# Kernel tuning notes

Hardware: AMD Instinct MI355X
Metric: run time of the kernel (lower is better)

Reference implementation:

```python
import jax, jax.numpy as jnp
from jax import lax
import numpy as np

GRID_SIZE = 3
SPLINE_ORDER = 2
N_BASIS = GRID_SIZE + SPLINE_ORDER  # 5
_H = 2.0 / GRID_SIZE  # grid_range [-1, 1]
# extended uniform grid, shape (1, grid_size + 2*spline_order + 1) = (1, 8)
GRID = (jnp.arange(-SPLINE_ORDER, GRID_SIZE + SPLINE_ORDER + 1, dtype=jnp.float32) * _H - 1.0)[None, :]


def b_splines(x):
    """Cox-de Boor B-spline bases. x: (..., F) -> (..., F, N_BASIS)."""
    x = x[..., None]
    g = GRID
    bases = ((x >= g[:, :-1]) & (x < g[:, 1:])).astype(x.dtype)
    for p in range(1, SPLINE_ORDER + 1):
        left = (x - g[:, :-(p + 1)]) / (g[:, p:-1] - g[:, :-(p + 1)])
        right = (g[:, p + 1:] - x) / (g[:, p + 1:] - g[:, 1:-p])
        bases = left * bases[..., :-1] + right * bases[..., 1:]
    return bases


def kan_conv(x, base_w, spline_w, scaler):
    """Unfold-based KAN conv: x NCHW -> NCHW. base_w (O,F), spline_w (O,F,K), scaler (O,F)."""
    # patches: (B, C*kh*kw, H', W'), channel-major feature ordering like torch unfold
    p = lax.conv_general_dilated_patches(x, (4, 4), (2, 2), ((1, 1), (1, 1)))
    f = jnp.transpose(p, (0, 2, 3, 1))  # (B, H', W', F)
    base = jax.nn.relu(f) @ base_w.T
    spl = jnp.einsum('bhwfk,ofk->bhwo', b_splines(f), spline_w * scaler[..., None])
    return jnp.transpose(base + spl, (0, 3, 1, 2))


def batchnorm(x, gamma, beta):
    # train-mode BN over (B,H,W) per channel, eps=1e-5 (torch default)
    m = x.mean((0, 2, 3), keepdims=True)
    v = x.var((0, 2, 3), keepdims=True)
    return (x - m) * lax.rsqrt(v + 1e-5) * gamma[None, :, None, None] + beta[None, :, None, None]


def setup_inputs() -> dict:
    key = jax.random.key(0)
    ks = jax.random.split(key, 32)
    B = 512
    chans = [(3, 32), (32, 64), (64, 128), (128, 128)]
    inp = {"x": jax.random.normal(ks[0], (B, 3, 32, 32), jnp.float32)}
    i = 1
    for li, (cin, cout) in enumerate(chans, start=1):
        F = cin * 16
        inp[f"bw{li}"] = jax.random.normal(ks[i], (cout, F), jnp.float32) * (0.8 / np.sqrt(F)); i += 1
        inp[f"sw{li}"] = jax.random.normal(ks[i], (cout, F, N_BASIS), jnp.float32) * (0.8 / np.sqrt(F)); i += 1
        inp[f"sc{li}"] = jnp.ones((cout, F), jnp.float32) + 0.05 * jax.random.normal(ks[i], (cout, F), jnp.float32); i += 1
    for bi, c in [(1, 64), (2, 128), (3, 128)]:
        inp[f"g{bi}"] = jnp.ones((c,), jnp.float32)
        inp[f"b{bi}"] = jnp.zeros((c,), jnp.float32)
    inp["fc_w"] = jax.random.normal(ks[i], (1, 128), jnp.float32) * (1.0 / np.sqrt(128)); i += 1
    inp["fc_b"] = jnp.zeros((1,), jnp.float32)
    return inp


def reference(x, bw1, sw1, sc1, bw2, sw2, sc2, bw3, sw3, sc3, bw4, sw4, sc4,
              g1, b1, g2, b2, g3, b3, fc_w, fc_b):
    h = kan_conv(x, bw1, sw1, sc1)                     # (B,32,16,16)
    h = kan_conv(h, bw2, sw2, sc2)                     # (B,64,8,8)
    h = batchnorm(h, g1, b1)
    h = kan_conv(h, bw3, sw3, sc3)                     # (B,128,4,4)
    h = batchnorm(h, g2, b2)
    h = kan_conv(h, bw4, sw4, sc4)                     # (B,128,2,2)
    h = batchnorm(h, g3, b3)
    h = h.mean((2, 3))                                 # AdaptiveAvgPool2d(1) + Flatten -> (B,128)
    return jax.nn.sigmoid(h @ fc_w.T + fc_b)           # (B,1)
```

## Files before the change

### kernel.cpp

```cpp
#include <hip/hip_runtime.h>
#include <hip/hip_bf16.h>
#include <math.h>

#define DEVINL __device__ __forceinline__

typedef short short8 __attribute__((ext_vector_type(8)));
typedef float f32x4 __attribute__((ext_vector_type(4)));

DEVINL unsigned short f2bf(float f) {
    union { float f; unsigned int u; } c; c.f = f;
    unsigned int u = c.u;
    return (unsigned short)((u + 0x7fffu + ((u >> 16) & 1u)) >> 16);
}

DEVINL unsigned int packbf2(float a, float b) {
    union { __hip_bfloat162 h; unsigned int u; } c;
    c.h = __float22bfloat162_rn(make_float2(a, b));
    return c.u;
}

DEVINL void gload_lds16(const unsigned int* g, unsigned int* l) {
    __builtin_amdgcn_global_load_lds((const __attribute__((address_space(1))) unsigned int*)g,
                                     (__attribute__((address_space(3))) unsigned int*)l, 16, 0, 0);
}

DEVINL uint4 expand_frag(float v) {
    float relu = fmaxf(v, 0.f);
    float u = fmaf(v, 1.5f, 3.5f);
    float fj = floorf(u);
    int j = (int)fj;
    float t = u - fj;
    float omt = 1.f - t;
    float v2 = 0.5f * omt * omt;
    float v1 = fmaf(t, omt, 0.5f);
    float v0 = 0.5f * t * t;
    float b[5];
#pragma unroll
    for (int i = 0; i < 5; ++i)
        b[i] = (i == j) ? v0 : (i == j - 1) ? v1 : (i == j - 2) ? v2 : 0.f;
    uint4 r;
    r.x = packbf2(relu, b[0]);
    r.y = packbf2(b[1], b[2]);
    r.z = packbf2(b[3], b[4]);
    r.w = 0u;
    return r;
}

DEVINL void prep_frag(int fi, int F, int NTT, const float* __restrict__ bw,
                      const float* __restrict__ sw, const float* __restrict__ sc,
                      unsigned short* __restrict__ wf) {
    int lane = fi & 63;
    int t = fi >> 6;
    int ks = t & 3;
    int t2 = t >> 2;
    int nt = t2 % NTT;
    int c = t2 / NTT;
    int tap = ks * 4 + (lane >> 4);
    int f = c * 16 + tap;
    int o = nt * 16 + (lane & 15);
    float scv = sc[o * F + f];
    float b = bw[o * F + f];
    float s0 = sw[(o * F + f) * 5 + 0] * scv;
    float s1 = sw[(o * F + f) * 5 + 1] * scv;
    float s2 = sw[(o * F + f) * 5 + 2] * scv;
    float s3 = sw[(o * F + f) * 5 + 3] * scv;
    float s4 = sw[(o * F + f) * 5 + 4] * scv;
    uint4 r;
    r.x = packbf2(b, s0);
    r.y = packbf2(s1, s2);
    r.z = packbf2(s3, s4);
    r.w = 0u;
    *(uint4*)&wf[(size_t)fi * 8] = r;
}

__global__ __launch_bounds__(256) void prep_all(
    const float* __restrict__ bw1, const float* __restrict__ sw1, const float* __restrict__ sc1,
    const float* __restrict__ bw2, const float* __restrict__ sw2, const float* __restrict__ sc2,
    const float* __restrict__ bw3, const float* __restrict__ sw3, const float* __restrict__ sc3,
    const float* __restrict__ bw4, const float* __restrict__ sw4, const float* __restrict__ sc4,
    unsigned short* __restrict__ wf1, unsigned short* __restrict__ wf2,
    unsigned short* __restrict__ wf3, unsigned short* __restrict__ wf4) {
    int fi = blockIdx.x * 256 + threadIdx.x;
    const int N1 = 3 * 32 * 16;
    const int N2 = 32 * 64 * 16;
    const int N3 = 64 * 128 * 16;
    const int N4 = 128 * 128 * 16;
    if (fi < N1) prep_frag(fi, 48, 2, bw1, sw1, sc1, wf1);
    else if (fi < N1 + N2) prep_frag(fi - N1, 512, 4, bw2, sw2, sc2, wf2);
    else if (fi < N1 + N2 + N3) prep_frag(fi - N1 - N2, 1024, 8, bw3, sw3, sc3, wf3);
    else if (fi < N1 + N2 + N3 + N4) prep_frag(fi - N1 - N2 - N3, 2048, 8, bw4, sw4, sc4, wf4);
}

template <int CIN, int COUTT, int NSP, int HOUT, int WOUT, int WM, int WN, int MT,
          int CPS, int UB, bool HASBN, int BNS, int NBN, bool SPLITOUT, int RPAD>
__global__ __launch_bounds__(256) void kan_conv_fused(
    const float* __restrict__ in, const unsigned short* __restrict__ wf,
    const float* __restrict__ part, const float* __restrict__ gamma,
    const float* __restrict__ beta, float* __restrict__ out) {
    constexpr int HIN = HOUT * 2, WIN = WOUT * 2, W2 = WOUT;
    constexpr int COUT = COUTT / NSP;
    constexpr int NTT = COUTT / 16;
    constexpr int NT = COUT / 16;
    constexpr int NTW = NT / WN;
    constexpr int BM = WM * MT * 16;
    constexpr int IMG_POS = HOUT * WOUT;
    constexpr int NIMG = BM / IMG_POS;
    constexpr int RS = WIN + RPAD;
    constexpr int IMG_STRIDE = HIN * RS + 1;
    constexpr int ASLOTS = NIMG * IMG_STRIDE + 1;
    constexpr int M_TOT = 512 * IMG_POS;
    constexpr int EV = NIMG * HIN * WIN;
    constexpr int EITER = (EV + 255) / 256;
    static_assert(WM * WN == 4, "4 waves");
    static_assert(CPS % UB == 0, "UB divides CPS");

    __shared__ uint4 A_e[UB][ASLOTS];
    __shared__ uint4 B_l[UB][COUT * 16];

    const int tid = threadIdx.x;
    const int lane = tid & 63;
    const int w = tid >> 6;
    const int wm = w % WM;
    const int wn = w / WM;
    const int g = lane >> 4;
    const int r16 = lane & 15;
    const int m0 = blockIdx.x * BM;
    const int b0 = m0 / IMG_POS;
    const int nh = (NSP > 1) ? ((int)blockIdx.y % NSP) : 0;
    const int kslice = (NSP > 1) ? ((int)blockIdx.y / NSP) : (SPLITOUT ? (int)blockIdx.y : 0);
    const int c0 = SPLITOUT ? kslice * CPS : 0;

    int aoff[MT];
    int vmask = 0;
#pragma unroll
    for (int mt = 0; mt < MT; ++mt) {
        int p = (wm * MT + mt) * 16 + r16;
        int m = m0 + p;
        int ow = m % WOUT;
        int oh = (m / WOUT) % HOUT;
        int bl = p / IMG_POS;
        int iw = 2 * ow - 1 + g;
        bool iv = (iw >= 0) && (iw < WIN);
        aoff[mt] = 1 + bl * IMG_STRIDE + (2 * oh) * RS + (iw & 1) * W2 + (iw >> 1);
#pragma unroll
        for (int ks = 0; ks < 4; ++ks) {
            bool vv = iv && !(oh == 0 && ks == 0) && !(oh == HOUT - 1 && ks == 3);
            vmask |= (vv ? 1 : 0) << (mt * 4 + ks);
        }
    }

    if (tid < UB) A_e[tid][0] = expand_frag(0.f);

    f32x4 acc[MT][NTW];
#pragma unroll
    for (int mt = 0; mt < MT; ++mt)
#pragma unroll
        for (int n = 0; n < NTW; ++n) acc[mt][n] = f32x4{0.f, 0.f, 0.f, 0.f};

    for (int cc = 0; cc < CPS; cc += UB) {
#pragma unroll
        for (int u = 0; u < UB; ++u) {
            const int ch = c0 + cc + u;
            const unsigned int* bsrc = (const unsigned int*)wf + ((size_t)ch * NTT + nh * NT) * 1024;
            unsigned int* bdst = (unsigned int*)&B_l[u][0];
#pragma unroll
            for (int r2 = 0; r2 < NT; ++r2)
                gload_lds16(bsrc + (r2 << 10) + tid * 4, bdst + (r2 << 10) + tid * 4);
        }
#pragma unroll
        for (int u = 0; u < UB; ++u) {
            const int ch = c0 + cc + u;
            float bsc = 1.f, bsh = 0.f;
            if (HASBN) {
                if constexpr (BNS == 1) {
                    bsc = part[ch * 2];
                    bsh = part[ch * 2 + 1];
                } else {
                    float sm = 0.f, s2 = 0.f;
#pragma unroll 4
                    for (int s = 0; s < BNS; ++s) {
                        sm += part[(ch * BNS + s) * 2];
                        s2 += part[(ch * BNS + s) * 2 + 1];
                    }
                    const float invN = 1.f / (float)NBN;
                    float mean = sm * invN;
                    float var = s2 * invN - mean * mean;
                    float rs = rsqrtf(var + 1e-5f);
                    bsc = gamma[ch] * rs;
                    bsh = beta[ch] - mean * bsc;
                }
            }
#pragma unroll
            for (int ii = 0; ii < EITER; ++ii) {
                int e = tid + ii * 256;
                if ((EV % 256 == 0) || e < EV) {
                    int bl = e / (HIN * WIN);
                    int r = e - bl * (HIN * WIN);
                    int ih = r / WIN;
                    int iw = r - ih * WIN;
                    float v = in[(((size_t)(b0 + bl) * CIN + ch) * HIN + ih) * WIN + iw];
                    if (HASBN) v = fmaf(v, bsc, bsh);
                    A_e[u][1 + bl * IMG_STRIDE + ih * RS + (iw & 1) * W2 + (iw >> 1)] = expand_frag(v);
                }
            }
        }
        __syncthreads();
#pragma unroll
        for (int u = 0; u < UB; ++u) {
#pragma unroll
            for (int ks = 0; ks < 4; ++ks) {
                short8 bf[NTW];
#pragma unroll
                for (int n = 0; n < NTW; ++n)
                    bf[n] = *(const short8*)&B_l[u][(((wn * NTW + n) * 4 + ks) << 6) + lane];
#pragma unroll
                for (int mt = 0; mt < MT; ++mt) {
                    int slot = ((vmask >> (mt * 4 + ks)) & 1) ? (aoff[mt] + (ks - 1) * RS) : 0;
                    short8 af = *(const short8*)&A_e[u][slot];
#pragma unroll
                    for (int n = 0; n < NTW; ++n)
                        acc[mt][n] = __builtin_amdgcn_mfma_f32_16x16x32_bf16(af, bf[n], acc[mt][n], 0, 0, 0);
                }
            }
        }
        __syncthreads();
    }

    const int colo = lane & 15;
    const int row4 = (lane >> 4) * 4;
#pragma unroll
    for (int mt = 0; mt < MT; ++mt) {
#pragma unroll
        for (int n = 0; n < NTW; ++n) {
            int o = nh * COUT + (wn * NTW + n) * 16 + colo;
#pragma unroll
            for (int rr = 0; rr < 4; ++rr) {
                int p = (wm * MT + mt) * 16 + row4 + rr;
                int m = m0 + p;
                if (SPLITOUT) {
                    out[((size_t)kslice * M_TOT + m) * COUTT + o] = acc[mt][n][rr];
                } else {
                    int ow = m % WOUT;
                    int t = m / WOUT;
                    int oh = t % HOUT;
                    int b = t / HOUT;
                    out[((b * COUTT + o) * HOUT + oh) * WOUT + ow] = acc[mt][n][rr];
                }
            }
        }
    }
}

template <int NS, int COUT, int HOUT, int WOUT, int NB>
__global__ __launch_bounds__(256) void reduce_bn(const float* __restrict__ P,
                                                 float* __restrict__ out,
                                                 float* __restrict__ part) {
    constexpr int M = 512 * HOUT * WOUT;
    static_assert(COUT == 128, "LDS reduce assumes 128 channels");
    static_assert(NB * 256 * 4 == M * COUT, "exact cover");
    const int tid = threadIdx.x;
    const int idx4 = blockIdx.x * 256 + tid;
    f32x4 s = {0.f, 0.f, 0.f, 0.f};
#pragma unroll
    for (int i = 0; i < NS; ++i)
        s += *(const f32x4*)&P[(size_t)i * M * COUT + (size_t)idx4 * 4];
    int o0 = (idx4 * 4) % COUT;
    int m = (idx4 * 4) / COUT;
    int ow = m % WOUT;
    int t = m / WOUT;
    int oh = t % HOUT;
    int b = t / HOUT;
    float sm[4], sq[4];
#pragma unroll
    for (int q = 0; q < 4; ++q) {
        out[((b * COUT + o0 + q) * HOUT + oh) * WOUT + ow] = s[q];
        sm[q] = s[q];
        sq[q] = s[q] * s[q];
    }
    __shared__ float red[2][COUT][8];
    int gch = tid & 31, h = tid >> 5;
#pragma unroll
    for (int q = 0; q < 4; ++q) {
        red[0][gch * 4 + q][h] = sm[q];
        red[1][gch * 4 + q][h] = sq[q];
    }
    __syncthreads();
    int st = tid >> 7;
    int c = tid & 127;
    float v = 0.f;
#pragma unroll
    for (int k = 0; k < 8; ++k) v += red[st][c][k];
    part[((size_t)c * NB + blockIdx.x) * 2 + st] = v;
}

template <int NB, int NBN>
__global__ __launch_bounds__(256) void bn_finish(const float* __restrict__ part,
                                                 const float* __restrict__ gamma,
                                                 const float* __restrict__ beta,
                                                 float* __restrict__ fin) {
    int c = blockIdx.x;
    int tid = threadIdx.x;
    float sm = 0.f, s2 = 0.f;
    for (int i = tid; i < NB; i += 256) {
        sm += part[((size_t)c * NB + i) * 2];
        s2 += part[((size_t)c * NB + i) * 2 + 1];
    }
    __shared__ float r0[256], r1[256];
    r0[tid] = sm; r1[tid] = s2;
    __syncthreads();
    for (int off = 128; off > 0; off >>= 1) {
        if (tid < off) { r0[tid] += r0[tid + off]; r1[tid] += r1[tid + off]; }
        __syncthreads();
    }
    if (tid == 0) {
        const float invN = 1.f / (float)NBN;
        float mean = r0[0] * invN;
        float var = r1[0] * invN - mean * mean;
        float rs = rsqrtf(var + 1e-5f);
        float scl = gamma[c] * rs;
        fin[c * 2] = scl;
        fin[c * 2 + 1] = beta[c] - mean * scl;
    }
}

template <int C, int HW, int S>
__global__ __launch_bounds__(256) void bn_partial(const float* __restrict__ a,
                                                  float* __restrict__ part) {
    constexpr int BS = 512 / S;
    constexpr int H4 = HW / 4;
    int c = blockIdx.x / S, s = blockIdx.x % S;
    int tid = threadIdx.x;
    float sm = 0.f, s2 = 0.f;
    for (int i = tid; i < BS * H4; i += 256) {
        int b = i / H4, r = i - (i / H4) * H4;
        f32x4 v = *(const f32x4*)&a[(((size_t)(s * BS + b) * C + c) * HW) + r * 4];
#pragma unroll
        for (int q = 0; q < 4; ++q) { sm += v[q]; s2 += v[q] * v[q]; }
    }
    __shared__ float r0[256], r1[256];
    r0[tid] = sm; r1[tid] = s2;
    __syncthreads();
    for (int off = 128; off > 0; off >>= 1) {
        if (tid < off) { r0[tid] += r0[tid + off]; r1[tid] += r1[tid + off]; }
        __syncthreads();
    }
    if (tid == 0) {
        part[(c * S + s) * 2] = r0[0];
        part[(c * S + s) * 2 + 1] = r1[0];
    }
}

__global__ void head_ker(const float* __restrict__ a4, const float* __restrict__ fin3,
                         const float* __restrict__ fcw, const float* __restrict__ fcb,
                         float* __restrict__ out) {
    int b = blockIdx.x;
    int lane = threadIdx.x;
    float acc = 0.0f;
#pragma unroll
    for (int j = 0; j < 2; ++j) {
        int o = lane + 64 * j;
        float scl = fin3[o * 2];
        float sh = fin3[o * 2 + 1];
        const float* p = a4 + (b * 128 + o) * 4;
        float sv = p[0] + p[1] + p[2] + p[3];
        float pooled = fmaf(sv * 0.25f, scl, sh);
        acc = fmaf(pooled, fcw[o], acc);
    }
#pragma unroll
    for (int off = 32; off > 0; off >>= 1) acc += __shfl_down(acc, off);
    if (lane == 0) out[b] = 1.0f / (1.0f + expf(-(acc + fcb[0])));
}

extern "C" void kernel_launch(void* const* d_in, const int* in_sizes, int n_in,
                              void* d_out, int out_size, void* d_ws, size_t ws_size,
                              hipStream_t stream) {
    const float* x   = (const float*)d_in[0];
    const float* bw1 = (const float*)d_in[1];
    const float* sw1 = (const float*)d_in[2];
    const float* sc1 = (const float*)d_in[3];
    const float* bw2 = (const float*)d_in[4];
    const float* sw2 = (const float*)d_in[5];
    const float* sc2 = (const float*)d_in[6];
    const float* bw3 = (const float*)d_in[7];
    const float* sw3 = (const float*)d_in[8];
    const float* sc3 = (const float*)d_in[9];
    const float* bw4 = (const float*)d_in[10];
    const float* sw4 = (const float*)d_in[11];
    const float* sc4 = (const float*)d_in[12];
    const float* g1  = (const float*)d_in[13];
    const float* b1  = (const float*)d_in[14];
    const float* g2  = (const float*)d_in[15];
    const float* b2  = (const float*)d_in[16];
    const float* g3  = (const float*)d_in[17];
    const float* b3  = (const float*)d_in[18];
    const float* fcw = (const float*)d_in[19];
    const float* fcb = (const float*)d_in[20];

    float* ws = (float*)d_ws;
    float* a1 = ws;
    float* a2 = a1 + 4194304;
    float* a3 = a2 + 2097152;
    float* a4 = a3 + 1048576;
    unsigned short* wf1 = (unsigned short*)(a4 + 262144);
    unsigned short* wf2 = wf1 + 12288;
    unsigned short* wf3 = wf2 + 262144;
    unsigned short* wf4 = wf3 + 1048576;
    float* part1 = (float*)(wf4 + 2097152);
    float* part2 = part1 + 2048;
    float* part3 = part2 + 262144;
    float* fin2  = part3 + 65536;
    float* fin3  = fin2 + 256;
    float* P3 = a1;
    float* P4 = a2;

    prep_all<<<1670, 256, 0, stream>>>(bw1, sw1, sc1, bw2, sw2, sc2,
                                       bw3, sw3, sc3, bw4, sw4, sc4,
                                       wf1, wf2, wf3, wf4);

    kan_conv_fused<3, 32, 1, 16, 16, 4, 1, 4, 3, 3, false, 1, 1, false, 0>
        <<<512, 256, 0, stream>>>(x, wf1, nullptr, nullptr, nullptr, a1);
    kan_conv_fused<32, 64, 2, 8, 8, 4, 1, 2, 32, 4, false, 1, 1, false, 0>
        <<<dim3(256, 2), 256, 0, stream>>>(a1, wf2, nullptr, nullptr, nullptr, a2);
    bn_partial<64, 64, 16><<<1024, 256, 0, stream>>>(a2, part1);
    kan_conv_fused<64, 128, 2, 4, 4, 4, 1, 2, 16, 2, true, 16, 32768, true, 1>
        <<<dim3(64, 8), 256, 0, stream>>>(a2, wf3, part1, g1, b1, P3);
    reduce_bn<4, 128, 4, 4, 1024><<<1024, 256, 0, stream>>>(P3, a3, part2);
    bn_finish<1024, 8192><<<128, 256, 0, stream>>>(part2, g2, b2, fin2);
    kan_conv_fused<128, 128, 2, 2, 2, 4, 1, 1, 16, 2, true, 1, 1, true, 0>
        <<<dim3(32, 16), 256, 0, stream>>>(a3, wf4, fin2, nullptr, nullptr, P4);
    reduce_bn<8, 128, 2, 2, 256><<<256, 256, 0, stream>>>(P4, a4, part3);
    bn_finish<256, 2048><<<128, 256, 0, stream>>>(part3, g3, b3, fin3);
    head_ker<<<512, 64, 0, stream>>>(a4, fin3, fcw, fcb, (float*)d_out);
}
```

Measured before the change: 131.8 us.

## Fuse BN1 statistics into conv2 epilogue and drop bn_partial pass

Conv2 now reduces per-channel sums and sums of squares from its accumulators into LDS and writes per-block partials. A small bn_finish kernel turns them into scale and shift, which conv3 consumes directly (BNS=1). This removes a separate pass that re-read the full conv2 output and stops conv3 from reducing 16 partials per channel itself. The cost is an extra LDS reduction and sync in the conv2 epilogue, plus one extra small kernel launch.

```diff
diff --git a/kernel.cpp b/kernel.cpp
--- a/kernel.cpp
+++ b/kernel.cpp
@@ -92,11 +92,13 @@
 }
 
 template <int CIN, int COUTT, int NSP, int HOUT, int WOUT, int WM, int WN, int MT,
-          int CPS, int UB, bool HASBN, int BNS, int NBN, bool SPLITOUT, int RPAD>
+          int CPS, int UB, bool HASBN, int BNS, int NBN, bool SPLITOUT, int RPAD,
+          bool STATS = false>
 __global__ __launch_bounds__(256) void kan_conv_fused(
     const float* __restrict__ in, const unsigned short* __restrict__ wf,
     const float* __restrict__ part, const float* __restrict__ gamma,
-    const float* __restrict__ beta, float* __restrict__ out) {
+    const float* __restrict__ beta, float* __restrict__ out,
+    float* __restrict__ statout) {
     constexpr int HIN = HOUT * 2, WIN = WOUT * 2, W2 = WOUT;
     constexpr int COUT = COUTT / NSP;
     constexpr int NTT = COUTT / 16;
@@ -113,6 +115,8 @@
     constexpr int EITER = (EV + 255) / 256;
     static_assert(WM * WN == 4, "4 waves");
     static_assert(CPS % UB == 0, "UB divides CPS");
+    static_assert(!STATS || WN == 1, "stats assumes WN==1 (16 contributors/channel)");
+    static_assert(!STATS || 2 * COUT <= 256, "stats reduce fits one block");
 
     __shared__ uint4 A_e[UB][ASLOTS];
     __shared__ uint4 B_l[UB][COUT * 16];
@@ -249,6 +253,34 @@
             }
         }
     }
+
+    if constexpr (STATS) {
+        float* red = (float*)&A_e[0][0];
+        const int contrib = wm * 4 + (lane >> 4);
+#pragma unroll
+        for (int n = 0; n < NTW; ++n) {
+            float ls = 0.f, ls2 = 0.f;
+#pragma unroll
+            for (int mt = 0; mt < MT; ++mt)
+#pragma unroll
+                for (int rr = 0; rr < 4; ++rr) {
+                    float v = acc[mt][n][rr];
+                    ls += v;
+                    ls2 += v * v;
+                }
+            int o = n * 16 + colo;
+            red[o * 16 + contrib] = ls;
+            red[(COUT + o) * 16 + contrib] = ls2;
+        }
+        __syncthreads();
+        if (tid < 2 * COUT) {
+            int st = tid / COUT, o = tid % COUT;
+            float v = 0.f;
+#pragma unroll
+            for (int k = 0; k < 16; ++k) v += red[(st * COUT + o) * 16 + k];
+            statout[(((size_t)(nh * COUT + o)) * gridDim.x + blockIdx.x) * 2 + st] = v;
+        }
+    }
 }
 
 template <int NS, int COUT, int HOUT, int WOUT, int NB>
@@ -320,33 +352,6 @@
         float scl = gamma[c] * rs;
         fin[c * 2] = scl;
         fin[c * 2 + 1] = beta[c] - mean * scl;
-    }
-}
-
-template <int C, int HW, int S>
-__global__ __launch_bounds__(256) void bn_partial(const float* __restrict__ a,
-                                                  float* __restrict__ part) {
-    constexpr int BS = 512 / S;
-    constexpr int H4 = HW / 4;
-    int c = blockIdx.x / S, s = blockIdx.x % S;
-    int tid = threadIdx.x;
-    float sm = 0.f, s2 = 0.f;
-    for (int i = tid; i < BS * H4; i += 256) {
-        int b = i / H4, r = i - (i / H4) * H4;
-        f32x4 v = *(const f32x4*)&a[(((size_t)(s * BS + b) * C + c) * HW) + r * 4];
-#pragma unroll
-        for (int q = 0; q < 4; ++q) { sm += v[q]; s2 += v[q] * v[q]; }
-    }
-    __shared__ float r0[256], r1[256];
-    r0[tid] = sm; r1[tid] = s2;
-    __syncthreads();
-    for (int off = 128; off > 0; off >>= 1) {
-        if (tid < off) { r0[tid] += r0[tid + off]; r1[tid] += r1[tid + off]; }
-        __syncthreads();
-    }
-    if (tid == 0) {
-        part[(c * S + s) * 2] = r0[0];
-        part[(c * S + s) * 2 + 1] = r1[0];
     }
 }
 
@@ -406,9 +411,10 @@
     unsigned short* wf3 = wf2 + 262144;
     unsigned short* wf4 = wf3 + 1048576;
     float* part1 = (float*)(wf4 + 2097152);
-    float* part2 = part1 + 2048;
+    float* part2 = part1 + 32768;
     float* part3 = part2 + 262144;
-    float* fin2  = part3 + 65536;
+    float* fin1  = part3 + 65536;
+    float* fin2  = fin1 + 128;
     float* fin3  = fin2 + 256;
     float* P3 = a1;
     float* P4 = a2;
@@ -418,16 +424,16 @@
                                        wf1, wf2, wf3, wf4);
 
     kan_conv_fused<3, 32, 1, 16, 16, 4, 1, 4, 3, 3, false, 1, 1, false, 0>
-        <<<512, 256, 0, stream>>>(x, wf1, nullptr, nullptr, nullptr, a1);
-    kan_conv_fused<32, 64, 2, 8, 8, 4, 1, 2, 32, 4, false, 1, 1, false, 0>
-        <<<dim3(256, 2), 256, 0, stream>>>(a1, wf2, nullptr, nullptr, nullptr, a2);
-    bn_partial<64, 64, 16><<<1024, 256, 0, stream>>>(a2, part1);
-    kan_conv_fused<64, 128, 2, 4, 4, 4, 1, 2, 16, 2, true, 16, 32768, true, 1>
-        <<<dim3(64, 8), 256, 0, stream>>>(a2, wf3, part1, g1, b1, P3);
+        <<<512, 256, 0, stream>>>(x, wf1, nullptr, nullptr, nullptr, a1, nullptr);
+    kan_conv_fused<32, 64, 2, 8, 8, 4, 1, 2, 32, 4, false, 1, 1, false, 0, true>
+        <<<dim3(256, 2), 256, 0, stream>>>(a1, wf2, nullptr, nullptr, nullptr, a2, part1);
+    bn_finish<256, 32768><<<64, 256, 0, stream>>>(part1, g1, b1, fin1);
+    kan_conv_fused<64, 128, 2, 4, 4, 4, 1, 2, 16, 2, true, 1, 1, true, 1>
+        <<<dim3(64, 8), 256, 0, stream>>>(a2, wf3, fin1, nullptr, nullptr, P3, nullptr);
     reduce_bn<4, 128, 4, 4, 1024><<<1024, 256, 0, stream>>>(P3, a3, part2);
     bn_finish<1024, 8192><<<128, 256, 0, stream>>>(part2, g2, b2, fin2);
     kan_conv_fused<128, 128, 2, 2, 2, 4, 1, 1, 16, 2, true, 1, 1, true, 0>
-        <<<dim3(32, 16), 256, 0, stream>>>(a3, wf4, fin2, nullptr, nullptr, P4);
+        <<<dim3(32, 16), 256, 0, stream>>>(a3, wf4, fin2, nullptr, nullptr, P4, nullptr);
     reduce_bn<8, 128, 2, 2, 256><<<256, 256, 0, stream>>>(P4, a4, part3);
     bn_finish<256, 2048><<<128, 256, 0, stream>>>(part3, g3, b3, fin3);
     head_ker<<<512, 64, 0, stream>>>(a4, fin3, fcw, fcb, (float*)d_out);
```

New measurement: 123.5 us. 6.3% less time.
